# Performance work log

Measured on AMD Instinct MI355X. Metric: run time of the kernel, lower is better.

## Reference

```python
import jax, jax.numpy as jnp
import numpy as np

N = 25000      # n_nodes
K = 16         # k_sparse (out-degree per node)
E = N * K      # n_edges
D = 12         # depth
U = 48         # units
FEATS = 2
EF = 1
EPS = 1e-5     # BatchNorm eps


def _lin(h, W, b):
    return h @ W.T + b


def _bn(h, g, b):
    # training-mode BatchNorm over dim 0 (biased variance, like torch)
    m = h.mean(0)
    v = jnp.mean((h - m) ** 2, axis=0)
    return (h - m) * jax.lax.rsqrt(v + EPS) * g + b


def setup_inputs():
    key = jax.random.key(0)
    ks = iter(jax.random.split(key, 64))

    def nrm(shape, fan):
        return jax.random.normal(next(ks), shape, dtype=jnp.float32) * float(1.0 / np.sqrt(fan))

    inp = {}
    inp['x'] = jax.random.uniform(next(ks), (N, FEATS), dtype=jnp.float32)
    inp['edge_attr'] = jax.random.uniform(next(ks), (E, EF), dtype=jnp.float32)
    src = jnp.repeat(jnp.arange(N, dtype=jnp.int32), K)            # each node has K out-edges
    dst = jax.random.randint(next(ks), (E,), 0, N, dtype=jnp.int32)
    inp['edge_index'] = jnp.stack([src, dst])                       # [2, E]
    inp['v_lin0_W'] = nrm((U, FEATS), FEATS); inp['v_lin0_b'] = nrm((U,), FEATS)
    for nm in ['vW1', 'vW2', 'vW3', 'vW4']:
        inp[nm] = nrm((D, U, U), U)
    for nm in ['vb1', 'vb2', 'vb3', 'vb4']:
        inp[nm] = nrm((D, U), U)
    inp['vbn_g'] = jnp.ones((D, U), jnp.float32); inp['vbn_b'] = jnp.zeros((D, U), jnp.float32)
    inp['e_lin0_W'] = nrm((U, EF), EF); inp['e_lin0_b'] = nrm((U,), EF)
    inp['eW'] = nrm((D, U, U), U); inp['eb'] = nrm((D, U), U)
    inp['ebn_g'] = jnp.ones((D, U), jnp.float32); inp['ebn_b'] = jnp.zeros((D, U), jnp.float32)
    inp['pW0'] = nrm((U, U), U); inp['pb0'] = nrm((U,), U)
    inp['pW1'] = nrm((U, U), U); inp['pb1'] = nrm((U,), U)
    inp['pW2'] = nrm((1, U), U); inp['pb2'] = nrm((1,), U)
    inp['zW0'] = nrm((U, U), U); inp['zb0'] = nrm((U,), U)
    inp['zW1'] = nrm((1, U), U); inp['zb1'] = nrm((1,), U)
    inp['k_sparse'] = K
    return inp


def _forward(edge_index, k_sparse, x, edge_attr, v_lin0_W, v_lin0_b, vW1, vb1, vW2, vb2, vW3, vb3, vW4, vb4, vbn_g, vbn_b, e_lin0_W, e_lin0_b, eW, eb, ebn_g, ebn_b, pW0, pb0, pW1, pb1, pW2, pb2, zW0, zb0, zW1, zb1):
    n = x.shape[0]
    src, dst = edge_index[0], edge_index[1]
    deg = jnp.maximum(jax.ops.segment_sum(jnp.ones((src.shape[0],), x.dtype), src, num_segments=n), 1.0)
    h = jax.nn.silu(_lin(x, v_lin0_W, v_lin0_b))          # [N, U]
    w = jax.nn.silu(_lin(edge_attr, e_lin0_W, e_lin0_b))  # [E, U]

    def layer(carry, p):
        h, w = carry
        W1, b1, W2, b2, W3, b3, W4, b4, gv, bv, We, be, ge, bee = p
        h1 = _lin(h, W1, b1); h2 = _lin(h, W2, b2)
        h3 = _lin(h, W3, b3); h4 = _lin(h, W4, b4)
        msg = jax.nn.sigmoid(w) * h2[dst]                                 # [E, U] gather + gate
        agg = jax.ops.segment_sum(msg, src, num_segments=n) / deg[:, None]  # scatter-mean to source node
        h_new = h + jax.nn.silu(_bn(h1 + agg, gv, bv))
        w_new = w + jax.nn.silu(_bn(_lin(w, We, be) + h3[src] + h4[dst], ge, bee))
        return (h_new, w_new), None

    (_, w), _ = jax.lax.scan(layer, (h, w), (vW1, vb1, vW2, vb2, vW3, vb3, vW4, vb4, vbn_g, vbn_b, eW, eb, ebn_g, ebn_b))

    # ParNet heuristic head: MLP then group-softmax over k_sparse edges per node
    p = jax.nn.silu(_lin(w, pW0, pb0))
    p = jax.nn.silu(_lin(p, pW1, pb1))
    p = _lin(p, pW2, pb2).reshape(-1, k_sparse)
    heu = jax.nn.softmax(p, axis=1).reshape(-1)                            # [E]
    # Z_net logZ head (mean over edges)
    logZ = jnp.mean(jax.nn.relu(_lin(w, zW0, zb0)) @ zW1.T + zb1, axis=0)  # [1]
    return heu, logZ


def reference(x, edge_attr, edge_index, v_lin0_W, v_lin0_b, vW1, vb1, vW2, vb2, vW3, vb3, vW4, vb4, vbn_g, vbn_b, e_lin0_W, e_lin0_b, eW, eb, ebn_g, ebn_b, pW0, pb0, pW1, pb1, pW2, pb2, zW0, zb0, zW1, zb1, k_sparse):
    return _forward(edge_index, k_sparse, x, edge_attr, v_lin0_W, v_lin0_b, vW1, vb1, vW2, vb2, vW3, vb3, vW4, vb4, vbn_g, vbn_b, e_lin0_W, e_lin0_b, eW, eb, ebn_g, ebn_b, pW0, pb0, pW1, pb1, pW2, pb2, zW0, zb0, zW1, zb1)
```

## Files before the change

kernel.cpp:

```cpp
#include <hip/hip_runtime.h>
#include <hip/hip_bf16.h>

#define NN 25000
#define KK 16
#define EE 400000
#define DD 12
#define UU 48
#define EPSBN 1e-5f
#define RP 88

using bf16 = __hip_bfloat16;
typedef short bf16x8 __attribute__((ext_vector_type(8)));
typedef float f32x4 __attribute__((ext_vector_type(4)));

__device__ __forceinline__ float b2f(bf16 v){ return __bfloat162float(v); }
__device__ __forceinline__ float sigm(float x){ return 1.f/(1.f+__expf(-x)); }
__device__ __forceinline__ float siluf(float x){ return x/(1.f+__expf(-x)); }
__device__ __forceinline__ short f2bs(float f){ bf16 h=__float2bfloat16(f); return *(short*)&h; }
__device__ __forceinline__ float bs2f(short s){ bf16 h; *(short*)&h = s; return __bfloat162float(h); }

__device__ __forceinline__ float ldx(const void* p, size_t i, bool isb){
  return isb ? b2f(((const bf16*)p)[i]) : ((const float*)p)[i];
}
__device__ __forceinline__ void stout(void* p, size_t i, float v, bool isb){
  if (isb) ((bf16*)p)[i] = __float2bfloat16(v);
  else     ((float*)p)[i] = v;
}
__device__ __forceinline__ bool dflag(const void* vbng){
  return *((const unsigned*)vbng) == 0x3F803F80u;
}
#define LDSFENCE() asm volatile("s_waitcnt lgkmcnt(0)" ::: "memory")

__global__ void k_init_nodes(const void* __restrict__ x, const void* __restrict__ W0,
                             const void* __restrict__ b0, float* __restrict__ h,
                             float* __restrict__ stats, float* __restrict__ zpart,
                             const void* __restrict__ fl){
  const bool isb = dflag(fl);
  int gid = blockIdx.x*256 + threadIdx.x;
  if (gid < DD*12288) stats[gid] = 0.f;
  if (gid < 64) zpart[gid] = 0.f;
  if (gid < NN*UU){
    int n = gid/UU, c = gid%UU;
    float acc = ldx(b0,c,isb) + ldx(W0,c*2,isb)*ldx(x,n*2,isb) + ldx(W0,c*2+1,isb)*ldx(x,n*2+1,isb);
    h[gid] = siluf(acc);
  }
}

__global__ void k_init_edges(const void* __restrict__ ea, const void* __restrict__ W0,
                             const void* __restrict__ b0, float* __restrict__ w,
                             const void* __restrict__ fl){
  const bool isb = dflag(fl);
  int gid = blockIdx.x*256 + threadIdx.x;
  if (gid < EE*UU){
    int e = gid/UU, c = gid%UU;
    float acc = ldx(b0,c,isb) + ldx(W0,c,isb)*ldx(ea,e,isb);
    w[gid] = siluf(acc);
  }
}

__global__ __launch_bounds__(256) void k_node(
    float* __restrict__ h, float* __restrict__ h1,
    short* __restrict__ h2b, short* __restrict__ h3b, short* __restrict__ h4b,
    const void* __restrict__ W1, const void* __restrict__ W2,
    const void* __restrict__ W3, const void* __restrict__ W4,
    const void* __restrict__ b1, const void* __restrict__ b2,
    const void* __restrict__ b3, const void* __restrict__ b4,
    const void* __restrict__ gv, const void* __restrict__ bv,
    const float* __restrict__ stats, int ctl, const void* __restrict__ fl)
{
  const bool isb = dflag(fl);
  const int d = ctl>>1, apply = ctl&1;
  const size_t WOFF = (size_t)d*UU*UU, BOFF = (size_t)d*UU;
  __shared__ alignas(16) short BT[4][48*RP];
  __shared__ alignas(16) short AT[4][16*RP];
  __shared__ float bL[4][UU];
  __shared__ float scV[96];
  __shared__ float sred[96];
  int tid = threadIdx.x, lane = tid&63, wid = tid>>6;
  const void* Ws[4] = {W1,W2,W3,W4};
  const void* bs[4] = {b1,b2,b3,b4};
  for (int i=tid;i<4*2304;i+=256){ int m=i/2304, j=i%2304; int r=j/48,k=j%48;
    BT[m][r*RP+k]=f2bs(ldx(Ws[m],WOFF+j,isb)); }
  for (int i=tid;i<4*768;i+=256){ int m=i/768, j=i%768; int r=j/16,k=48+(j%16); BT[m][r*RP+k]=0; }
  for (int i=tid;i<4*256;i+=256){ int wv=i/256, j=i%256; int r=j/16,k=48+(j%16); AT[wv][r*RP+k]=0; }
  if (tid<192) bL[tid/48][tid%48] = ldx(bs[tid/48],BOFF+(tid%48),isb);
  if (apply && tid<96){
    const float* sp = stats + (size_t)(d-1)*12288;
    float s=0.f;
    for (int k2=0;k2<64;k2++) s += sp[k2*96+tid];
    sred[tid]=s;
  }
  __syncthreads();
  if (apply && tid<48){
    float mean = sred[tid]/(float)NN;
    float var = sred[48+tid]/(float)NN - mean*mean; if (var<0.f) var=0.f;
    float sc = ldx(gv,(size_t)(d-1)*48+tid,isb) * rsqrtf(var+EPSBN);
    scV[tid]=sc; scV[48+tid]=ldx(bv,(size_t)(d-1)*48+tid,isb) - mean*sc;
  }
  __syncthreads();

  int quad = lane>>4, lrow = lane&15;
  short* A = AT[wid];
  int gw = blockIdx.x*4+wid, gws = gridDim.x*4;
  const int NT = (NN+15)/16;
  for (int t=gw; t<NT; t+=gws){
    int nb = t*16;
    #pragma unroll
    for (int j=0;j<3;j++){
      int f = lane+64*j; int r=f/12, c4=f%12; int n=nb+r;
      short4 s4; s4.x=0;s4.y=0;s4.z=0;s4.w=0;
      if (n<NN){
        size_t gi = (size_t)n*48 + c4*4;
        float4 hv = *(const float4*)&h[gi];
        if (apply){
          float4 yv = *(const float4*)&h1[gi];
          int c0=c4*4;
          hv.x += siluf(scV[c0+0]*yv.x + scV[48+c0+0]);
          hv.y += siluf(scV[c0+1]*yv.y + scV[48+c0+1]);
          hv.z += siluf(scV[c0+2]*yv.z + scV[48+c0+2]);
          hv.w += siluf(scV[c0+3]*yv.w + scV[48+c0+3]);
          *(float4*)&h[gi] = hv;
        }
        s4.x=f2bs(hv.x); s4.y=f2bs(hv.y); s4.z=f2bs(hv.z); s4.w=f2bs(hv.w);
      }
      *(short4*)&A[r*RP + c4*4] = s4;
    }
    LDSFENCE();
    bf16x8 a0 = *(const bf16x8*)&A[lrow*RP + quad*8];
    bf16x8 a1 = *(const bf16x8*)&A[lrow*RP + 32 + quad*8];
    #pragma unroll
    for (int m=0;m<4;m++){
      f32x4 ac0={0,0,0,0}, ac1={0,0,0,0}, ac2={0,0,0,0};
      bf16x8 bfr;
      bfr = *(const bf16x8*)&BT[m][(0+lrow)*RP + quad*8];      ac0=__builtin_amdgcn_mfma_f32_16x16x32_bf16(a0,bfr,ac0,0,0,0);
      bfr = *(const bf16x8*)&BT[m][(0+lrow)*RP + 32 + quad*8]; ac0=__builtin_amdgcn_mfma_f32_16x16x32_bf16(a1,bfr,ac0,0,0,0);
      bfr = *(const bf16x8*)&BT[m][(16+lrow)*RP + quad*8];     ac1=__builtin_amdgcn_mfma_f32_16x16x32_bf16(a0,bfr,ac1,0,0,0);
      bfr = *(const bf16x8*)&BT[m][(16+lrow)*RP + 32 + quad*8];ac1=__builtin_amdgcn_mfma_f32_16x16x32_bf16(a1,bfr,ac1,0,0,0);
      bfr = *(const bf16x8*)&BT[m][(32+lrow)*RP + quad*8];     ac2=__builtin_amdgcn_mfma_f32_16x16x32_bf16(a0,bfr,ac2,0,0,0);
      bfr = *(const bf16x8*)&BT[m][(32+lrow)*RP + 32 + quad*8];ac2=__builtin_amdgcn_mfma_f32_16x16x32_bf16(a1,bfr,ac2,0,0,0);
      #pragma unroll
      for (int nt=0;nt<3;nt++){
        int c = nt*16+lrow;
        f32x4 ac = (nt==0)?ac0:((nt==1)?ac1:ac2);
        float bv2 = bL[m][c];
        #pragma unroll
        for (int r=0;r<4;r++){
          int n = nb + quad*4 + r;
          if (n<NN){
            float v = ac[r] + bv2;
            if (m==0) h1[(size_t)n*48+c] = v;
            else if (m==1) h2b[(size_t)n*48+c] = f2bs(v);
            else if (m==2) h3b[(size_t)n*48+c] = f2bs(v);
            else           h4b[(size_t)n*48+c] = f2bs(v);
          }
        }
      }
    }
  }
}

__global__ __launch_bounds__(256) void k_edge(
    float* __restrict__ w, short* __restrict__ tmp,
    float* __restrict__ h1, const short* __restrict__ h2b,
    const short* __restrict__ h3b, const short* __restrict__ h4b,
    const int* __restrict__ dst,
    const void* __restrict__ We, const void* __restrict__ eb,
    const void* __restrict__ ge, const void* __restrict__ be,
    float* __restrict__ stats, int ctl, const void* __restrict__ fl)
{
  const bool isb = dflag(fl);
  const int d = ctl>>1, apply = ctl&1;
  const size_t WOFF = (size_t)d*UU*UU, BOFF = (size_t)d*UU;
  __shared__ alignas(16) short BT[48*RP];
  __shared__ alignas(16) short AT[4][16*RP];
  __shared__ float ebL[UU];
  __shared__ float scE[96];
  __shared__ float sred[96];
  __shared__ float sACC[4][192];
  int tid = threadIdx.x, lane = tid&63, wid = tid>>6;
  for (int i=tid;i<2304;i+=256){ int r=i/48,k=i%48; BT[r*RP+k]=f2bs(ldx(We,WOFF+i,isb)); }
  for (int i=tid;i<768;i+=256){ int r=i/16,k=48+(i%16); BT[r*RP+k]=0; }
  for (int i=tid;i<4*256;i+=256){ int wv=i/256, j=i%256; int r=j/16,k=48+(j%16); AT[wv][r*RP+k]=0; }
  if (tid<48) ebL[tid]=ldx(eb,BOFF+tid,isb);
  for (int i=tid;i<768;i+=256) ((float*)sACC)[i]=0.f;
  if (apply && tid<96){
    const float* sp = stats + (size_t)(d-1)*12288 + 6144;
    float s=0.f;
    for (int k2=0;k2<64;k2++) s += sp[k2*96+tid];
    sred[tid]=s;
  }
  __syncthreads();
  if (apply && tid<48){
    float mean = sred[tid]/(float)EE;
    float var = sred[48+tid]/(float)EE - mean*mean; if (var<0.f) var=0.f;
    float sc = ldx(ge,(size_t)(d-1)*48+tid,isb) * rsqrtf(var+EPSBN);
    scE[tid]=sc; scE[48+tid]=ldx(be,(size_t)(d-1)*48+tid,isb) - mean*sc;
  }
  __syncthreads();

  int quad = lane>>4, lrow = lane&15;
  short* A = AT[wid];
  float* myStats = stats + (size_t)d*12288;
  float accY[3]={0,0,0}, accY2[3]={0,0,0}, accT[3]={0,0,0}, accT2[3]={0,0,0};
  int gw = blockIdx.x*4+wid, gws = gridDim.x*4;
  for (int n=gw; n<NN; n+=gws){
    size_t basef = (size_t)n*768;
    #pragma unroll
    for (int j=0;j<3;j++){
      int f = lane+64*j; int r=f/12, c4=f%12;
      size_t gi = basef + r*48 + c4*4;
      float4 wv = *(const float4*)&w[gi];
      if (apply){
        short4 t4 = *(const short4*)&tmp[gi];
        int c0=c4*4;
        wv.x += siluf(scE[c0+0]*bs2f(t4.x) + scE[48+c0+0]);
        wv.y += siluf(scE[c0+1]*bs2f(t4.y) + scE[48+c0+1]);
        wv.z += siluf(scE[c0+2]*bs2f(t4.z) + scE[48+c0+2]);
        wv.w += siluf(scE[c0+3]*bs2f(t4.w) + scE[48+c0+3]);
        *(float4*)&w[gi] = wv;
      }
      short4 s4; s4.x=f2bs(wv.x); s4.y=f2bs(wv.y); s4.z=f2bs(wv.z); s4.w=f2bs(wv.w);
      *(short4*)&A[r*RP + c4*4] = s4;
    }
    LDSFENCE();
    bf16x8 a0 = *(const bf16x8*)&A[lrow*RP + quad*8];
    bf16x8 a1 = *(const bf16x8*)&A[lrow*RP + 32 + quad*8];
    f32x4 ac0={0,0,0,0}, ac1={0,0,0,0}, ac2={0,0,0,0};
    bf16x8 bfr;
    bfr = *(const bf16x8*)&BT[(0+lrow)*RP + quad*8];      ac0=__builtin_amdgcn_mfma_f32_16x16x32_bf16(a0,bfr,ac0,0,0,0);
    bfr = *(const bf16x8*)&BT[(0+lrow)*RP + 32 + quad*8]; ac0=__builtin_amdgcn_mfma_f32_16x16x32_bf16(a1,bfr,ac0,0,0,0);
    bfr = *(const bf16x8*)&BT[(16+lrow)*RP + quad*8];     ac1=__builtin_amdgcn_mfma_f32_16x16x32_bf16(a0,bfr,ac1,0,0,0);
    bfr = *(const bf16x8*)&BT[(16+lrow)*RP + 32 + quad*8];ac1=__builtin_amdgcn_mfma_f32_16x16x32_bf16(a1,bfr,ac1,0,0,0);
    bfr = *(const bf16x8*)&BT[(32+lrow)*RP + quad*8];     ac2=__builtin_amdgcn_mfma_f32_16x16x32_bf16(a0,bfr,ac2,0,0,0);
    bfr = *(const bf16x8*)&BT[(32+lrow)*RP + 32 + quad*8];ac2=__builtin_amdgcn_mfma_f32_16x16x32_bf16(a1,bfr,ac2,0,0,0);
    int de[4];
    #pragma unroll
    for (int r=0;r<4;r++) de[r] = dst[n*16 + quad*4 + r];
    #pragma unroll
    for (int nt=0;nt<3;nt++){
      int c = nt*16+lrow;
      f32x4 ac = (nt==0)?ac0:((nt==1)?ac1:ac2);
      float bv = ebL[c];
      float h3v = bs2f(h3b[(size_t)n*48+c]);
      float pT=0.f, pT2=0.f, pM=0.f;
      #pragma unroll
      for (int r=0;r<4;r++){
        int e = quad*4+r;
        float t = ac[r] + bv + h3v + bs2f(h4b[(size_t)de[r]*48+c]);
        tmp[basef + e*48 + c] = f2bs(t);
        pT += t; pT2 += t*t;
        float wv = bs2f(A[e*RP+c]);
        pM += bs2f(h2b[(size_t)de[r]*48+c]) * sigm(wv);
      }
      pT  += __shfl_xor(pT,16);  pT  += __shfl_xor(pT,32);
      pT2 += __shfl_xor(pT2,16); pT2 += __shfl_xor(pT2,32);
      pM  += __shfl_xor(pM,16);  pM  += __shfl_xor(pM,32);
      accT[nt] += pT; accT2[nt] += pT2;
      if (lane<16){
        float yv = h1[(size_t)n*48+c] + pM*(1.f/16.f);
        h1[(size_t)n*48+c] = yv;
        accY[nt] += yv; accY2[nt] += yv*yv;
      }
    }
  }
  if (lane<16){
    #pragma unroll
    for (int nt=0;nt<3;nt++){
      int c = nt*16+lane;
      sACC[wid][c]      = accY[nt];
      sACC[wid][48+c]   = accY2[nt];
      sACC[wid][96+c]   = accT[nt];
      sACC[wid][144+c]  = accT2[nt];
    }
  }
  __syncthreads();
  if (tid<192){
    float s = sACC[0][tid]+sACC[1][tid]+sACC[2][tid]+sACC[3][tid];
    int bk = (blockIdx.x&63)*96;
    if (tid<96) atomicAdd(&myStats[bk+tid], s);
    else        atomicAdd(&myStats[6144+bk+(tid-96)], s);
  }
}

__global__ __launch_bounds__(256) void k_head1(
    const float* __restrict__ w, short* __restrict__ tmp,
    const void* __restrict__ pW0, const void* __restrict__ pb0,
    const void* __restrict__ zW0, const void* __restrict__ zb0,
    const void* __restrict__ zW1,
    const void* __restrict__ ge, const void* __restrict__ be,
    const float* __restrict__ stats, float* __restrict__ zpart,
    const void* __restrict__ fl)
{
  const bool isb = dflag(fl);
  __shared__ alignas(16) short BT0[48*RP];
  __shared__ alignas(16) short BT1[48*RP];
  __shared__ alignas(16) short AT[4][16*RP];
  __shared__ float pb0L[UU], zb0L[UU], zW1L[UU];
  __shared__ float scE[96];
  __shared__ float sred[96];
  __shared__ float zS[4];
  int tid = threadIdx.x, lane = tid&63, wid = tid>>6;
  for (int i=tid;i<2304;i+=256){ int r=i/48,k=i%48;
    BT0[r*RP+k]=f2bs(ldx(pW0,i,isb)); BT1[r*RP+k]=f2bs(ldx(zW0,i,isb)); }
  for (int i=tid;i<768;i+=256){ int r=i/16,k=48+(i%16); BT0[r*RP+k]=0; BT1[r*RP+k]=0; }
  for (int i=tid;i<4*256;i+=256){ int wv=i/256, j=i%256; int r=j/16,k=48+(j%16); AT[wv][r*RP+k]=0; }
  if (tid<48){ pb0L[tid]=ldx(pb0,tid,isb); zb0L[tid]=ldx(zb0,tid,isb); zW1L[tid]=ldx(zW1,tid,isb); }
  if (tid<96){
    const float* sp = stats + (size_t)(DD-1)*12288 + 6144;
    float s=0.f;
    for (int k2=0;k2<64;k2++) s += sp[k2*96+tid];
    sred[tid]=s;
  }
  __syncthreads();
  if (tid<48){
    float mean = sred[tid]/(float)EE;
    float var = sred[48+tid]/(float)EE - mean*mean; if (var<0.f) var=0.f;
    float sc = ldx(ge,(size_t)(DD-1)*48+tid,isb) * rsqrtf(var+EPSBN);
    scE[tid]=sc; scE[48+tid]=ldx(be,(size_t)(DD-1)*48+tid,isb) - mean*sc;
  }
  __syncthreads();

  int quad = lane>>4, lrow = lane&15;
  short* A = AT[wid];
  float zacc = 0.f;
  int gw = blockIdx.x*4+wid, gws = gridDim.x*4;
  for (int n=gw; n<NN; n+=gws){
    size_t basef = (size_t)n*768;
    #pragma unroll
    for (int j=0;j<3;j++){
      int f = lane+64*j; int r=f/12, c4=f%12;
      size_t gi = basef + r*48 + c4*4;
      float4 wv = *(const float4*)&w[gi];
      short4 t4 = *(const short4*)&tmp[gi];
      int c0=c4*4;
      wv.x += siluf(scE[c0+0]*bs2f(t4.x) + scE[48+c0+0]);
      wv.y += siluf(scE[c0+1]*bs2f(t4.y) + scE[48+c0+1]);
      wv.z += siluf(scE[c0+2]*bs2f(t4.z) + scE[48+c0+2]);
      wv.w += siluf(scE[c0+3]*bs2f(t4.w) + scE[48+c0+3]);
      short4 s4; s4.x=f2bs(wv.x); s4.y=f2bs(wv.y); s4.z=f2bs(wv.z); s4.w=f2bs(wv.w);
      *(short4*)&A[r*RP + c4*4] = s4;
    }
    LDSFENCE();
    bf16x8 a0 = *(const bf16x8*)&A[lrow*RP + quad*8];
    bf16x8 a1 = *(const bf16x8*)&A[lrow*RP + 32 + quad*8];
    f32x4 p0={0,0,0,0}, p1={0,0,0,0}, p2={0,0,0,0};
    f32x4 z0={0,0,0,0}, z1={0,0,0,0}, z2={0,0,0,0};
    bf16x8 bfr;
    bfr=*(const bf16x8*)&BT0[(0+lrow)*RP+quad*8];       p0=__builtin_amdgcn_mfma_f32_16x16x32_bf16(a0,bfr,p0,0,0,0);
    bfr=*(const bf16x8*)&BT0[(0+lrow)*RP+32+quad*8];    p0=__builtin_amdgcn_mfma_f32_16x16x32_bf16(a1,bfr,p0,0,0,0);
    bfr=*(const bf16x8*)&BT0[(16+lrow)*RP+quad*8];      p1=__builtin_amdgcn_mfma_f32_16x16x32_bf16(a0,bfr,p1,0,0,0);
    bfr=*(const bf16x8*)&BT0[(16+lrow)*RP+32+quad*8];   p1=__builtin_amdgcn_mfma_f32_16x16x32_bf16(a1,bfr,p1,0,0,0);
    bfr=*(const bf16x8*)&BT0[(32+lrow)*RP+quad*8];      p2=__builtin_amdgcn_mfma_f32_16x16x32_bf16(a0,bfr,p2,0,0,0);
    bfr=*(const bf16x8*)&BT0[(32+lrow)*RP+32+quad*8];   p2=__builtin_amdgcn_mfma_f32_16x16x32_bf16(a1,bfr,p2,0,0,0);
    bfr=*(const bf16x8*)&BT1[(0+lrow)*RP+quad*8];       z0=__builtin_amdgcn_mfma_f32_16x16x32_bf16(a0,bfr,z0,0,0,0);
    bfr=*(const bf16x8*)&BT1[(0+lrow)*RP+32+quad*8];    z0=__builtin_amdgcn_mfma_f32_16x16x32_bf16(a1,bfr,z0,0,0,0);
    bfr=*(const bf16x8*)&BT1[(16+lrow)*RP+quad*8];      z1=__builtin_amdgcn_mfma_f32_16x16x32_bf16(a0,bfr,z1,0,0,0);
    bfr=*(const bf16x8*)&BT1[(16+lrow)*RP+32+quad*8];   z1=__builtin_amdgcn_mfma_f32_16x16x32_bf16(a1,bfr,z1,0,0,0);
    bfr=*(const bf16x8*)&BT1[(32+lrow)*RP+quad*8];      z2=__builtin_amdgcn_mfma_f32_16x16x32_bf16(a0,bfr,z2,0,0,0);
    bfr=*(const bf16x8*)&BT1[(32+lrow)*RP+32+quad*8];   z2=__builtin_amdgcn_mfma_f32_16x16x32_bf16(a1,bfr,z2,0,0,0);
    #pragma unroll
    for (int nt=0;nt<3;nt++){
      int c = nt*16+lrow;
      f32x4 pp = (nt==0)?p0:((nt==1)?p1:p2);
      f32x4 zz = (nt==0)?z0:((nt==1)?z1:z2);
      float pb = pb0L[c], zb = zb0L[c], zw = zW1L[c];
      #pragma unroll
      for (int r=0;r<4;r++){
        int e = quad*4+r;
        A[e*RP+c] = f2bs(siluf(pp[r] + pb));
        float zr = zz[r] + zb;
        zacc += zw * (zr > 0.f ? zr : 0.f);
      }
    }
    LDSFENCE();
    #pragma unroll
    for (int j=0;j<2;j++){
      int idx = lane + 64*j;
      if (idx < 96){
        int r = idx/6, c8 = idx%6;
        *(bf16x8*)&tmp[basef + r*48 + c8*8] = *(const bf16x8*)&A[r*RP + c8*8];
      }
    }
  }
  zacc += __shfl_xor(zacc,1); zacc += __shfl_xor(zacc,2); zacc += __shfl_xor(zacc,4);
  zacc += __shfl_xor(zacc,8); zacc += __shfl_xor(zacc,16); zacc += __shfl_xor(zacc,32);
  if (lane==0) zS[wid]=zacc;
  __syncthreads();
  if (tid==0) atomicAdd(&zpart[blockIdx.x&63], zS[0]+zS[1]+zS[2]+zS[3]);
}

__global__ __launch_bounds__(256) void k_head2(
    const short* __restrict__ tmp,
    const void* __restrict__ pW1, const void* __restrict__ pb1,
    const void* __restrict__ pW2,
    void* __restrict__ out, const void* __restrict__ fl)
{
  const bool isb = dflag(fl);
  __shared__ alignas(16) short BT[48*RP];
  __shared__ alignas(16) short AT[4][16*RP];
  __shared__ float pb1L[UU], pW2L[UU];
  int tid = threadIdx.x, lane = tid&63, wid = tid>>6;
  for (int i=tid;i<2304;i+=256){ int r=i/48,k=i%48; BT[r*RP+k]=f2bs(ldx(pW1,i,isb)); }
  for (int i=tid;i<768;i+=256){ int r=i/16,k=48+(i%16); BT[r*RP+k]=0; }
  for (int i=tid;i<4*256;i+=256){ int wv=i/256, j=i%256; int r=j/16,k=48+(j%16); AT[wv][r*RP+k]=0; }
  if (tid<48){ pb1L[tid]=ldx(pb1,tid,isb); pW2L[tid]=ldx(pW2,tid,isb); }
  __syncthreads();

  int quad = lane>>4, lrow = lane&15;
  short* A = AT[wid];
  int gw = blockIdx.x*4+wid, gws = gridDim.x*4;
  for (int n=gw; n<NN; n+=gws){
    size_t basef = (size_t)n*768;
    #pragma unroll
    for (int j=0;j<2;j++){
      int idx = lane + 64*j;
      if (idx < 96){
        int r = idx/6, c8 = idx%6;
        *(bf16x8*)&A[r*RP + c8*8] = *(const bf16x8*)&tmp[basef + r*48 + c8*8];
      }
    }
    LDSFENCE();
    bf16x8 a0 = *(const bf16x8*)&A[lrow*RP + quad*8];
    bf16x8 a1 = *(const bf16x8*)&A[lrow*RP + 32 + quad*8];
    f32x4 q0={0,0,0,0}, q1={0,0,0,0}, q2={0,0,0,0};
    bf16x8 bfr;
    bfr=*(const bf16x8*)&BT[(0+lrow)*RP+quad*8];       q0=__builtin_amdgcn_mfma_f32_16x16x32_bf16(a0,bfr,q0,0,0,0);
    bfr=*(const bf16x8*)&BT[(0+lrow)*RP+32+quad*8];    q0=__builtin_amdgcn_mfma_f32_16x16x32_bf16(a1,bfr,q0,0,0,0);
    bfr=*(const bf16x8*)&BT[(16+lrow)*RP+quad*8];      q1=__builtin_amdgcn_mfma_f32_16x16x32_bf16(a0,bfr,q1,0,0,0);
    bfr=*(const bf16x8*)&BT[(16+lrow)*RP+32+quad*8];   q1=__builtin_amdgcn_mfma_f32_16x16x32_bf16(a1,bfr,q1,0,0,0);
    bfr=*(const bf16x8*)&BT[(32+lrow)*RP+quad*8];      q2=__builtin_amdgcn_mfma_f32_16x16x32_bf16(a0,bfr,q2,0,0,0);
    bfr=*(const bf16x8*)&BT[(32+lrow)*RP+32+quad*8];   q2=__builtin_amdgcn_mfma_f32_16x16x32_bf16(a1,bfr,q2,0,0,0);
    float pp[4] = {0.f,0.f,0.f,0.f};
    #pragma unroll
    for (int nt=0;nt<3;nt++){
      int c = nt*16+lrow;
      f32x4 qq = (nt==0)?q0:((nt==1)?q1:q2);
      float pb = pb1L[c], pw = pW2L[c];
      #pragma unroll
      for (int r=0;r<4;r++) pp[r] += pw * siluf(qq[r] + pb);
    }
    #pragma unroll
    for (int r=0;r<4;r++){
      pp[r] += __shfl_xor(pp[r],1); pp[r] += __shfl_xor(pp[r],2);
      pp[r] += __shfl_xor(pp[r],4); pp[r] += __shfl_xor(pp[r],8);
    }
    float mx = fmaxf(fmaxf(pp[0],pp[1]), fmaxf(pp[2],pp[3]));
    mx = fmaxf(mx, __shfl_xor(mx,16)); mx = fmaxf(mx, __shfl_xor(mx,32));
    float ex[4]; float se = 0.f;
    #pragma unroll
    for (int r=0;r<4;r++){ ex[r] = __expf(pp[r]-mx); se += ex[r]; }
    se += __shfl_xor(se,16); se += __shfl_xor(se,32);
    float inv = 1.f/se;
    if (lrow==0){
      #pragma unroll
      for (int r=0;r<4;r++) stout(out, (size_t)n*16 + quad*4 + r, ex[r]*inv, isb);
    }
  }
}

__global__ void k_final(const float* __restrict__ zpart, const void* __restrict__ zb1,
                        void* __restrict__ out, const void* __restrict__ fl){
  const bool isb = dflag(fl);
  int tid=threadIdx.x;
  float s = (tid<64) ? zpart[tid] : 0.f;
  s += __shfl_xor(s,1); s += __shfl_xor(s,2); s += __shfl_xor(s,4);
  s += __shfl_xor(s,8); s += __shfl_xor(s,16); s += __shfl_xor(s,32);
  if (tid==0) stout(out, EE, s/(float)EE + ldx(zb1,0,isb), isb);
}

extern "C" void kernel_launch(void* const* d_in, const int* in_sizes, int n_in,
                              void* d_out, int out_size, void* d_ws, size_t ws_size,
                              hipStream_t stream){
  (void)in_sizes; (void)n_in; (void)out_size; (void)ws_size;
  const void* x=d_in[0]; const void* ea=d_in[1];
  const int* ei=(const int*)d_in[2];
  const void* vW0=d_in[3]; const void* vb0=d_in[4];
  const void* vW1=d_in[5]; const void* vW2=d_in[6]; const void* vW3=d_in[7]; const void* vW4=d_in[8];
  const void* vb1=d_in[9]; const void* vb2=d_in[10]; const void* vb3=d_in[11]; const void* vb4=d_in[12];
  const void* vbng=d_in[13]; const void* vbnb=d_in[14];
  const void* eW0=d_in[15]; const void* eb0=d_in[16];
  const void* eW=d_in[17]; const void* ebv=d_in[18];
  const void* ebng=d_in[19]; const void* ebnb=d_in[20];
  const void* pW0=d_in[21]; const void* pb0=d_in[22];
  const void* pW1=d_in[23]; const void* pb1=d_in[24];
  const void* pW2=d_in[25]; const void* pb2=d_in[26]; (void)pb2;
  const void* zW0=d_in[27]; const void* zb0=d_in[28];
  const void* zW1=d_in[29]; const void* zb1=d_in[30];
  const int* dst = ei + EE;
  const void* fl = vbng;

  float* h   = (float*)d_ws;
  float* h1  = h  + (size_t)NN*UU;
  short* h2b = (short*)(h1 + (size_t)NN*UU);
  short* h3b = h2b + (size_t)NN*UU;
  short* h4b = h3b + (size_t)NN*UU;
  float* w   = (float*)(h4b + (size_t)NN*UU);
  short* tmp = (short*)(w + (size_t)EE*UU);
  float* stats = (float*)(tmp + (size_t)EE*UU);
  float* zpart = stats + DD*12288;

  k_init_nodes<<<(NN*UU+255)/256,256,0,stream>>>(x,vW0,vb0,h,stats,zpart,fl);
  k_init_edges<<<(EE*UU+255)/256,256,0,stream>>>(ea,eW0,eb0,w,fl);
  for (int d=0; d<DD; d++){
    int ctl = (d<<1) | (d>0 ? 1 : 0);
    k_node<<<256,256,0,stream>>>(h,h1,h2b,h3b,h4b,
        vW1,vW2,vW3,vW4,vb1,vb2,vb3,vb4,vbng,vbnb,stats,ctl,fl);
    k_edge<<<1024,256,0,stream>>>(w,tmp,h1,h2b,h3b,h4b,dst,eW,ebv,ebng,ebnb,stats,ctl,fl);
  }
  k_head1<<<1024,256,0,stream>>>(w,tmp,pW0,pb0,zW0,zb0,zW1,ebng,ebnb,stats,zpart,fl);
  k_head2<<<1024,256,0,stream>>>(tmp,pW1,pb1,pW2,d_out,fl);
  k_final<<<1,64,0,stream>>>(zpart,zb1,d_out,fl);
}
```

Measured before the change: 1.422 ms.

## Store node projections in fp16, vectorize weight staging, retune grids

Node projection buffers (h2,h3,h4) and the edge pre-BN temporary switch from bf16 to fp16 storage, for more mantissa precision at the same size. Weight staging into LDS uses 16-byte vector copies when inputs are bf16, replacing per-element conversion. The dst index load is hoisted ahead of the MFMA so the gather address latency overlaps compute. k_head1 writes its output straight to global instead of bouncing through LDS, and k_node and k_edge launch with larger grids. Together these aim to cut setup and latency overhead and raise occupancy, at the cost of a narrower fp16 range for those intermediates.

Measured after the change: 1.417 ms. Within noise of the previous version (-0.4%).

```diff
diff --git a/kernel.cpp b/kernel.cpp
--- a/kernel.cpp
+++ b/kernel.cpp
@@ -1,5 +1,6 @@
 #include <hip/hip_runtime.h>
 #include <hip/hip_bf16.h>
+#include <hip/hip_fp16.h>
 
 #define NN 25000
 #define KK 16
@@ -18,6 +19,8 @@
 __device__ __forceinline__ float siluf(float x){ return x/(1.f+__expf(-x)); }
 __device__ __forceinline__ short f2bs(float f){ bf16 h=__float2bfloat16(f); return *(short*)&h; }
 __device__ __forceinline__ float bs2f(short s){ bf16 h; *(short*)&h = s; return __bfloat162float(h); }
+__device__ __forceinline__ short f2hs(float f){ __half h=__float2half(f); return *(short*)&h; }
+__device__ __forceinline__ float hs2f(short s){ __half h; *(short*)&h = s; return __half2float(h); }
 
 __device__ __forceinline__ float ldx(const void* p, size_t i, bool isb){
   return isb ? b2f(((const bf16*)p)[i]) : ((const float*)p)[i];
@@ -30,6 +33,18 @@
   return *((const unsigned*)vbng) == 0x3F803F80u;
 }
 #define LDSFENCE() asm volatile("s_waitcnt lgkmcnt(0)" ::: "memory")
+
+__device__ __forceinline__ void stageW(short* BT, const void* W, size_t WOFF, bool isb, int tid){
+  if (isb){
+    const short* src = ((const short*)W) + WOFF;
+    for (int j=tid; j<288; j+=256){
+      int r=j/6, k=(j%6)*8;
+      *(bf16x8*)&BT[r*RP+k] = *(const bf16x8*)(src + j*8);
+    }
+  } else {
+    for (int i=tid;i<2304;i+=256){ int r=i/48,k=i%48; BT[r*RP+k]=f2bs(ldx(W,WOFF+i,false)); }
+  }
+}
 
 __global__ void k_init_nodes(const void* __restrict__ x, const void* __restrict__ W0,
                              const void* __restrict__ b0, float* __restrict__ h,
@@ -79,8 +94,8 @@
   int tid = threadIdx.x, lane = tid&63, wid = tid>>6;
   const void* Ws[4] = {W1,W2,W3,W4};
   const void* bs[4] = {b1,b2,b3,b4};
-  for (int i=tid;i<4*2304;i+=256){ int m=i/2304, j=i%2304; int r=j/48,k=j%48;
-    BT[m][r*RP+k]=f2bs(ldx(Ws[m],WOFF+j,isb)); }
+  #pragma unroll
+  for (int m=0;m<4;m++) stageW(BT[m], Ws[m], WOFF, isb, tid);
   for (int i=tid;i<4*768;i+=256){ int m=i/768, j=i%768; int r=j/16,k=48+(j%16); BT[m][r*RP+k]=0; }
   for (int i=tid;i<4*256;i+=256){ int wv=i/256, j=i%256; int r=j/16,k=48+(j%16); AT[wv][r*RP+k]=0; }
   if (tid<192) bL[tid/48][tid%48] = ldx(bs[tid/48],BOFF+(tid%48),isb);
@@ -149,9 +164,9 @@
           if (n<NN){
             float v = ac[r] + bv2;
             if (m==0) h1[(size_t)n*48+c] = v;
-            else if (m==1) h2b[(size_t)n*48+c] = f2bs(v);
-            else if (m==2) h3b[(size_t)n*48+c] = f2bs(v);
-            else           h4b[(size_t)n*48+c] = f2bs(v);
+            else if (m==1) h2b[(size_t)n*48+c] = f2hs(v);
+            else if (m==2) h3b[(size_t)n*48+c] = f2hs(v);
+            else           h4b[(size_t)n*48+c] = f2hs(v);
           }
         }
       }
@@ -178,7 +193,7 @@
   __shared__ float sred[96];
   __shared__ float sACC[4][192];
   int tid = threadIdx.x, lane = tid&63, wid = tid>>6;
-  for (int i=tid;i<2304;i+=256){ int r=i/48,k=i%48; BT[r*RP+k]=f2bs(ldx(We,WOFF+i,isb)); }
+  stageW(BT, We, WOFF, isb, tid);
   for (int i=tid;i<768;i+=256){ int r=i/16,k=48+(i%16); BT[r*RP+k]=0; }
   for (int i=tid;i<4*256;i+=256){ int wv=i/256, j=i%256; int r=j/16,k=48+(j%16); AT[wv][r*RP+k]=0; }
   if (tid<48) ebL[tid]=ldx(eb,BOFF+tid,isb);
@@ -205,6 +220,9 @@
   int gw = blockIdx.x*4+wid, gws = gridDim.x*4;
   for (int n=gw; n<NN; n+=gws){
     size_t basef = (size_t)n*768;
+    int de[4];
+    #pragma unroll
+    for (int r=0;r<4;r++) de[r] = dst[n*16 + quad*4 + r];
     #pragma unroll
     for (int j=0;j<3;j++){
       int f = lane+64*j; int r=f/12, c4=f%12;
@@ -213,10 +231,10 @@
       if (apply){
         short4 t4 = *(const short4*)&tmp[gi];
         int c0=c4*4;
-        wv.x += siluf(scE[c0+0]*bs2f(t4.x) + scE[48+c0+0]);
-        wv.y += siluf(scE[c0+1]*bs2f(t4.y) + scE[48+c0+1]);
-        wv.z += siluf(scE[c0+2]*bs2f(t4.z) + scE[48+c0+2]);
-        wv.w += siluf(scE[c0+3]*bs2f(t4.w) + scE[48+c0+3]);
+        wv.x += siluf(scE[c0+0]*hs2f(t4.x) + scE[48+c0+0]);
+        wv.y += siluf(scE[c0+1]*hs2f(t4.y) + scE[48+c0+1]);
+        wv.z += siluf(scE[c0+2]*hs2f(t4.z) + scE[48+c0+2]);
+        wv.w += siluf(scE[c0+3]*hs2f(t4.w) + scE[48+c0+3]);
         *(float4*)&w[gi] = wv;
       }
       short4 s4; s4.x=f2bs(wv.x); s4.y=f2bs(wv.y); s4.z=f2bs(wv.z); s4.w=f2bs(wv.w);
@@ -233,24 +251,21 @@
     bfr = *(const bf16x8*)&BT[(16+lrow)*RP + 32 + quad*8];ac1=__builtin_amdgcn_mfma_f32_16x16x32_bf16(a1,bfr,ac1,0,0,0);
     bfr = *(const bf16x8*)&BT[(32+lrow)*RP + quad*8];     ac2=__builtin_amdgcn_mfma_f32_16x16x32_bf16(a0,bfr,ac2,0,0,0);
     bfr = *(const bf16x8*)&BT[(32+lrow)*RP + 32 + quad*8];ac2=__builtin_amdgcn_mfma_f32_16x16x32_bf16(a1,bfr,ac2,0,0,0);
-    int de[4];
-    #pragma unroll
-    for (int r=0;r<4;r++) de[r] = dst[n*16 + quad*4 + r];
     #pragma unroll
     for (int nt=0;nt<3;nt++){
       int c = nt*16+lrow;
       f32x4 ac = (nt==0)?ac0:((nt==1)?ac1:ac2);
       float bv = ebL[c];
-      float h3v = bs2f(h3b[(size_t)n*48+c]);
+      float h3v = hs2f(h3b[(size_t)n*48+c]);
       float pT=0.f, pT2=0.f, pM=0.f;
       #pragma unroll
       for (int r=0;r<4;r++){
         int e = quad*4+r;
-        float t = ac[r] + bv + h3v + bs2f(h4b[(size_t)de[r]*48+c]);
-        tmp[basef + e*48 + c] = f2bs(t);
+        float t = ac[r] + bv + h3v + hs2f(h4b[(size_t)de[r]*48+c]);
+        tmp[basef + e*48 + c] = f2hs(t);
         pT += t; pT2 += t*t;
-        float wv = bs2f(A[e*RP+c]);
-        pM += bs2f(h2b[(size_t)de[r]*48+c]) * sigm(wv);
+        float gate = bs2f(A[e*RP+c]);
+        pM += hs2f(h2b[(size_t)de[r]*48+c]) * sigm(gate);
       }
       pT  += __shfl_xor(pT,16);  pT  += __shfl_xor(pT,32);
       pT2 += __shfl_xor(pT2,16); pT2 += __shfl_xor(pT2,32);
@@ -300,8 +315,8 @@
   __shared__ float sred[96];
   __shared__ float zS[4];
   int tid = threadIdx.x, lane = tid&63, wid = tid>>6;
-  for (int i=tid;i<2304;i+=256){ int r=i/48,k=i%48;
-    BT0[r*RP+k]=f2bs(ldx(pW0,i,isb)); BT1[r*RP+k]=f2bs(ldx(zW0,i,isb)); }
+  stageW(BT0, pW0, 0, isb, tid);
+  stageW(BT1, zW0, 0, isb, tid);
   for (int i=tid;i<768;i+=256){ int r=i/16,k=48+(i%16); BT0[r*RP+k]=0; BT1[r*RP+k]=0; }
   for (int i=tid;i<4*256;i+=256){ int wv=i/256, j=i%256; int r=j/16,k=48+(j%16); AT[wv][r*RP+k]=0; }
   if (tid<48){ pb0L[tid]=ldx(pb0,tid,isb); zb0L[tid]=ldx(zb0,tid,isb); zW1L[tid]=ldx(zW1,tid,isb); }
@@ -333,10 +348,10 @@
       float4 wv = *(const float4*)&w[gi];
       short4 t4 = *(const short4*)&tmp[gi];
       int c0=c4*4;
-      wv.x += siluf(scE[c0+0]*bs2f(t4.x) + scE[48+c0+0]);
-      wv.y += siluf(scE[c0+1]*bs2f(t4.y) + scE[48+c0+1]);
-      wv.z += siluf(scE[c0+2]*bs2f(t4.z) + scE[48+c0+2]);
-      wv.w += siluf(scE[c0+3]*bs2f(t4.w) + scE[48+c0+3]);
+      wv.x += siluf(scE[c0+0]*hs2f(t4.x) + scE[48+c0+0]);
+      wv.y += siluf(scE[c0+1]*hs2f(t4.y) + scE[48+c0+1]);
+      wv.z += siluf(scE[c0+2]*hs2f(t4.z) + scE[48+c0+2]);
+      wv.w += siluf(scE[c0+3]*hs2f(t4.w) + scE[48+c0+3]);
       short4 s4; s4.x=f2bs(wv.x); s4.y=f2bs(wv.y); s4.z=f2bs(wv.z); s4.w=f2bs(wv.w);
       *(short4*)&A[r*RP + c4*4] = s4;
     }
@@ -367,18 +382,9 @@
       #pragma unroll
       for (int r=0;r<4;r++){
         int e = quad*4+r;
-        A[e*RP+c] = f2bs(siluf(pp[r] + pb));
+        tmp[basef + e*48 + c] = f2bs(siluf(pp[r] + pb));
         float zr = zz[r] + zb;
         zacc += zw * (zr > 0.f ? zr : 0.f);
-      }
-    }
-    LDSFENCE();
-    #pragma unroll
-    for (int j=0;j<2;j++){
-      int idx = lane + 64*j;
-      if (idx < 96){
-        int r = idx/6, c8 = idx%6;
-        *(bf16x8*)&tmp[basef + r*48 + c8*8] = *(const bf16x8*)&A[r*RP + c8*8];
       }
     }
   }
@@ -400,7 +406,7 @@
   __shared__ alignas(16) short AT[4][16*RP];
   __shared__ float pb1L[UU], pW2L[UU];
   int tid = threadIdx.x, lane = tid&63, wid = tid>>6;
-  for (int i=tid;i<2304;i+=256){ int r=i/48,k=i%48; BT[r*RP+k]=f2bs(ldx(pW1,i,isb)); }
+  stageW(BT, pW1, 0, isb, tid);
   for (int i=tid;i<768;i+=256){ int r=i/16,k=48+(i%16); BT[r*RP+k]=0; }
   for (int i=tid;i<4*256;i+=256){ int wv=i/256, j=i%256; int r=j/16,k=48+(j%16); AT[wv][r*RP+k]=0; }
   if (tid<48){ pb1L[tid]=ldx(pb1,tid,isb); pW2L[tid]=ldx(pW2,tid,isb); }
@@ -503,9 +509,9 @@
   k_init_edges<<<(EE*UU+255)/256,256,0,stream>>>(ea,eW0,eb0,w,fl);
   for (int d=0; d<DD; d++){
     int ctl = (d<<1) | (d>0 ? 1 : 0);
-    k_node<<<256,256,0,stream>>>(h,h1,h2b,h3b,h4b,
+    k_node<<<512,256,0,stream>>>(h,h1,h2b,h3b,h4b,
         vW1,vW2,vW3,vW4,vb1,vb2,vb3,vb4,vbng,vbnb,stats,ctl,fl);
-    k_edge<<<1024,256,0,stream>>>(w,tmp,h1,h2b,h3b,h4b,dst,eW,ebv,ebng,ebnb,stats,ctl,fl);
+    k_edge<<<1536,256,0,stream>>>(w,tmp,h1,h2b,h3b,h4b,dst,eW,ebv,ebng,ebnb,stats,ctl,fl);
   }
   k_head1<<<1024,256,0,stream>>>(w,tmp,pW0,pb0,zW0,zb0,zW1,ebng,ebnb,stats,zpart,fl);
   k_head2<<<1024,256,0,stream>>>(tmp,pW1,pb1,pW2,d_out,fl);
```
